# Performance work log

Hardware: AMD Instinct MI355X
Metric: run time of the kernel (lower is better)

The kernel has to match this reference:

```python
import jax, jax.numpy as jnp
import numpy as np

HIDDEN = 1024
HEADS = 16
HEAD_DIM = HIDDEN // HEADS
EPS = 1e-5


def setup_inputs() -> dict:
    key = jax.random.key(0)
    ks = jax.random.split(key, 9)
    B, S, H = 2, 2048, HIDDEN
    scale = 1.0 / np.sqrt(H)
    inp = {
        "hidden_states": jax.random.normal(ks[0], (B, S, H), dtype=jnp.float32),
        "Wq": jax.random.normal(ks[1], (H, H), dtype=jnp.float32) * scale,
        "bq": jnp.zeros((H,), jnp.float32),
        "Wk": jax.random.normal(ks[2], (H, H), dtype=jnp.float32) * scale,
        "bk": jnp.zeros((H,), jnp.float32),
        "Wv": jax.random.normal(ks[3], (H, H), dtype=jnp.float32) * scale,
        "bv": jnp.zeros((H,), jnp.float32),
        "Wo": jax.random.normal(ks[4], (H, H), dtype=jnp.float32) * scale,
        "bo": jnp.zeros((H,), jnp.float32),
        "gamma": jnp.ones((H,), jnp.float32),
        "beta": jnp.zeros((H,), jnp.float32),
    }
    return inp


def reference(hidden_states, Wq, bq, Wk, bk, Wv, bv, Wo, bo, gamma, beta):
    B, S, H = hidden_states.shape
    residual = hidden_states

    def shape(x):  # [B,S,H] -> [B,heads,S,head_dim]
        return x.reshape(B, S, HEADS, HEAD_DIM).transpose(0, 2, 1, 3)

    q = shape(hidden_states @ Wq + bq)
    k = shape(hidden_states @ Wk + bk)
    v = shape(hidden_states @ Wv + bv)

    scores = jnp.einsum("bhqd,bhkd->bhqk", q, k) / jnp.sqrt(
        jnp.asarray(HEAD_DIM, hidden_states.dtype))
    probs = jax.nn.softmax(scores, axis=-1)
    context = jnp.einsum("bhqk,bhkd->bhqd", probs, v)
    context = context.transpose(0, 2, 1, 3).reshape(B, S, H)

    output = context @ Wo + bo
    x = output + residual
    mu = jnp.mean(x, axis=-1, keepdims=True)
    var = jnp.mean(jnp.square(x - mu), axis=-1, keepdims=True)
    return (x - mu) * jax.lax.rsqrt(var + EPS) * gamma + beta
```

## Files before the change

kernel.cpp:

```cpp
#include <hip/hip_runtime.h>
#include <hip/hip_bf16.h>
#include <math.h>

#define HIDDEN 1024
#define HEADS 16
#define HEAD_DIM 64
#define EPS 1e-5f

typedef __attribute__((ext_vector_type(8))) short bf16x8;
typedef __attribute__((ext_vector_type(4))) float f32x4;

#if defined(__has_builtin)
#if __has_builtin(__builtin_amdgcn_exp2f)
#define EXP2(x) __builtin_amdgcn_exp2f(x)
#endif
#endif
#ifndef EXP2
#define EXP2(x) exp2f(x)
#endif

#define QSCALE 0.18033688011112042f

__device__ __forceinline__ short f2bf(float f) {
    union { float f; unsigned u; } v; v.f = f;
    unsigned r = v.u + 0x7fffu + ((v.u >> 16) & 1u);
    return (short)(r >> 16);
}

__device__ __forceinline__ void gl_lds16(const void* g, void* l) {
    __builtin_amdgcn_global_load_lds(
        (const __attribute__((address_space(1))) void*)g,
        (__attribute__((address_space(3))) void*)l, 16, 0, 0);
}

__global__ __launch_bounds__(256) void cast_bf16_kernel(
    const float* __restrict__ in, short* __restrict__ out, int n)
{
    int i = (blockIdx.x * 256 + threadIdx.x) * 4;
    if (i >= n) return;
    float4 v = *(const float4*)(in + i);
    short o[4] = { f2bf(v.x), f2bf(v.y), f2bf(v.z), f2bf(v.w) };
    *(uint2*)(out + i) = *(uint2*)o;
}

__global__ __launch_bounds__(256) void wtrans_kernel(
    const float* __restrict__ Wq, const float* __restrict__ Wk,
    const float* __restrict__ Wv, const float* __restrict__ Wo,
    short* __restrict__ Wt3, short* __restrict__ Wot)
{
    const int wsel = blockIdx.z;
    const float* W = (wsel == 0) ? Wq : (wsel == 1) ? Wk : (wsel == 2) ? Wv : Wo;
    short* dst = (wsel < 3) ? (Wt3 + (size_t)wsel * 1024 * 1024) : Wot;
    const float scale = (wsel == 0) ? QSCALE : 1.0f;

    __shared__ short tile[32][33];
    int n0 = blockIdx.x * 32;
    int k0 = blockIdx.y * 32;
    int tx = threadIdx.x & 31;
    int ty = threadIdx.x >> 5;
    #pragma unroll
    for (int i = 0; i < 32; i += 8)
        tile[ty + i][tx] = f2bf(W[(size_t)(k0 + ty + i) * 1024 + n0 + tx] * scale);
    __syncthreads();
    #pragma unroll
    for (int i = 0; i < 32; i += 8)
        dst[(size_t)(n0 + ty + i) * 1024 + k0 + tx] = tile[tx][ty + i];
}

__global__ __launch_bounds__(256) void concat_bias_kernel(
    const float* __restrict__ bq, const float* __restrict__ bk,
    const float* __restrict__ bv, float* __restrict__ b3)
{
    int i = blockIdx.x * 256 + threadIdx.x;
    if (i >= 3072) return;
    float v = (i < 1024) ? bq[i] * QSCALE
            : (i < 2048) ? bk[i - 1024] : bv[i - 2048];
    b3[i] = v;
}

__global__ __launch_bounds__(256) void gemm_bt_mfma(
    const short* __restrict__ A, const short* __restrict__ Bt,
    const float* __restrict__ bias,
    void* __restrict__ C0, int ldc0,
    void* __restrict__ C1, int split_col, int ldc1,
    const float* __restrict__ resid,
    int M, int N, int K, int out_bf16)
{
    __shared__ short As[128 * 32];
    __shared__ short Bs[128 * 32];
    const int tid = threadIdx.x;
    const int wave = tid >> 6, lane = tid & 63;
    const int ln16 = lane & 15, quad = lane >> 4;
    const int wm = (wave >> 1) * 64, wn = (wave & 1) * 64;
    const int brow = blockIdx.y * 128, bcol = blockIdx.x * 128;

    const int sr  = lane >> 2;
    const int scb = lane & 3;

    f32x4 acc[4][4];
    #pragma unroll
    for (int mt = 0; mt < 4; ++mt)
        #pragma unroll
        for (int nt = 0; nt < 4; ++nt) acc[mt][nt] = (f32x4){0.f, 0.f, 0.f, 0.f};

    for (int k0 = 0; k0 < K; k0 += 32) {
        __syncthreads();
        #pragma unroll
        for (int i = 0; i < 2; ++i) {
            int rb = i * 64 + wave * 16;
            int r  = rb + sr;
            int csrc = (scb ^ ((r >> 1) & 3)) * 8;
            gl_lds16(A  + (size_t)(brow + r) * K + k0 + csrc, &As[rb * 32]);
            gl_lds16(Bt + (size_t)(bcol + r) * K + k0 + csrc, &Bs[rb * 32]);
        }
        __syncthreads();

        bf16x8 af[4], bf[4];
        #pragma unroll
        for (int mt = 0; mt < 4; ++mt) {
            int r = wm + mt * 16 + ln16;
            af[mt] = *(const bf16x8*)&As[r * 32 + ((quad ^ ((r >> 1) & 3)) * 8)];
        }
        #pragma unroll
        for (int nt = 0; nt < 4; ++nt) {
            int r = wn + nt * 16 + ln16;
            bf[nt] = *(const bf16x8*)&Bs[r * 32 + ((quad ^ ((r >> 1) & 3)) * 8)];
        }
        #pragma unroll
        for (int mt = 0; mt < 4; ++mt)
            #pragma unroll
            for (int nt = 0; nt < 4; ++nt)
                acc[mt][nt] = __builtin_amdgcn_mfma_f32_16x16x32_bf16(
                    af[mt], bf[nt], acc[mt][nt], 0, 0, 0);
    }

    void* Cp = C0; int ld = ldc0; int coff = 0;
    if (bcol >= split_col) { Cp = C1; ld = ldc1; coff = split_col; }

    #pragma unroll
    for (int mt = 0; mt < 4; ++mt) {
        #pragma unroll
        for (int r = 0; r < 4; ++r) {
            int row = brow + wm + mt * 16 + quad * 4 + r;
            #pragma unroll
            for (int nt = 0; nt < 4; ++nt) {
                int col = bcol + wn + nt * 16 + ln16;
                float v = acc[mt][nt][r] + bias[col];
                if (resid) v += resid[(size_t)row * N + col];
                if (out_bf16) ((short*)Cp)[(size_t)row * ld + (col - coff)] = f2bf(v);
                else          ((float*)Cp)[(size_t)row * ld + (col - coff)] = v;
            }
        }
    }
}

__global__ __launch_bounds__(256) void vtranspose_kernel(
    const short* __restrict__ Vb, short* __restrict__ VT)
{
    __shared__ short t[64][72];
    const int c0 = blockIdx.x * 64;
    const int r0 = blockIdx.y * 64;
    const int tid = threadIdx.x;
    #pragma unroll
    for (int i = 0; i < 2; ++i) {
        int idx = tid + i * 256;
        int r = idx >> 3, cc = (idx & 7) * 8;
        *(uint4*)&t[r][cc] = *(const uint4*)(Vb + (size_t)(r0 + r) * 1024 + c0 + cc);
    }
    __syncthreads();
    #pragma unroll
    for (int i = 0; i < 2; ++i) {
        int idx = tid + i * 256;
        int c = idx >> 3, rr = (idx & 7) * 8;
        short tmp[8];
        #pragma unroll
        for (int j = 0; j < 8; ++j) tmp[j] = t[rr + j][c];
        *(uint4*)(VT + (size_t)(c0 + c) * 4096 + r0 + rr) = *(uint4*)tmp;
    }
}

__global__ __launch_bounds__(256) void attn_mfma_kernel(
    const short* __restrict__ QKb, const short* __restrict__ VT,
    short* __restrict__ Ctx)
{
    const int S = 2048;
    const int h = blockIdx.x, qt = blockIdx.y, b = blockIdx.z;
    const int tid = threadIdx.x;
    const int wave = tid >> 6, lane = tid & 63;
    const int ln16 = lane & 15, quad = lane >> 4;

    __shared__ short Ks[64 * 64];
    __shared__ short Vs[64 * 64];
    __shared__ short Ps[128 * 72];

    const int q0 = qt * 128 + wave * 32;

    bf16x8 qfrag[2][2];
    #pragma unroll
    for (int qg = 0; qg < 2; ++qg)
        #pragma unroll
        for (int kb = 0; kb < 2; ++kb)
            qfrag[qg][kb] = *(const bf16x8*)(QKb +
                (size_t)(b * S + q0 + qg * 16 + ln16) * 2048 + h * 64 + kb * 32 + quad * 8);

    bf16x8 ones;
    #pragma unroll
    for (int j = 0; j < 8; ++j) ones[j] = (short)0x3F80;

    f32x4 of[2][4], lacc[2];
    #pragma unroll
    for (int qg = 0; qg < 2; ++qg) {
        lacc[qg] = (f32x4){0.f, 0.f, 0.f, 0.f};
        #pragma unroll
        for (int nt = 0; nt < 4; ++nt) of[qg][nt] = (f32x4){0.f, 0.f, 0.f, 0.f};
    }

    const int sr  = lane >> 3;
    const int scb = lane & 7;

    for (int kt = 0; kt < S / 64; ++kt) {
        __syncthreads();
        #pragma unroll
        for (int i = 0; i < 2; ++i) {
            int ci = wave * 2 + i;
            int r  = ci * 8 + sr;
            int csrc = ((scb ^ (r & 7))) * 8;
            gl_lds16(QKb + (size_t)(b * S + kt * 64 + r) * 2048 + 1024 + h * 64 + csrc,
                     &Ks[ci * 512]);
            gl_lds16(VT + (size_t)(h * 64 + r) * 4096 + b * S + kt * 64 + csrc,
                     &Vs[ci * 512]);
        }
        __syncthreads();

        #pragma unroll
        for (int nt = 0; nt < 4; ++nt) {
            bf16x8 kf[2];
            #pragma unroll
            for (int kb = 0; kb < 2; ++kb) {
                int r = nt * 16 + ln16;
                int cb = (kb * 4 + quad) ^ (r & 7);
                kf[kb] = *(const bf16x8*)&Ks[r * 64 + cb * 8];
            }
            #pragma unroll
            for (int qg = 0; qg < 2; ++qg) {
                f32x4 a = (f32x4){0.f, 0.f, 0.f, 0.f};
                a = __builtin_amdgcn_mfma_f32_16x16x32_bf16(kf[0], qfrag[qg][0], a, 0, 0, 0);
                a = __builtin_amdgcn_mfma_f32_16x16x32_bf16(kf[1], qfrag[qg][1], a, 0, 0, 0);
                float p0 = EXP2(a[0]), p1 = EXP2(a[1]);
                float p2 = EXP2(a[2]), p3 = EXP2(a[3]);
                union { __hip_bfloat162 h2; unsigned u; } c01, c23;
                c01.h2 = __float22bfloat162_rn(make_float2(p0, p1));
                c23.h2 = __float22bfloat162_rn(make_float2(p2, p3));
                uint2 w; w.x = c01.u; w.y = c23.u;
                *(uint2*)&Ps[(wave * 32 + qg * 16 + ln16) * 72 + nt * 16 + quad * 4] = w;
            }
        }

        bf16x8 pf[2][2];
        #pragma unroll
        for (int qg = 0; qg < 2; ++qg)
            #pragma unroll
            for (int kb = 0; kb < 2; ++kb)
                pf[qg][kb] = *(const bf16x8*)
                    &Ps[(wave * 32 + qg * 16 + ln16) * 72 + kb * 32 + quad * 8];

        #pragma unroll
        for (int qg = 0; qg < 2; ++qg) {
            lacc[qg] = __builtin_amdgcn_mfma_f32_16x16x32_bf16(pf[qg][0], ones, lacc[qg], 0, 0, 0);
            lacc[qg] = __builtin_amdgcn_mfma_f32_16x16x32_bf16(pf[qg][1], ones, lacc[qg], 0, 0, 0);
        }
        #pragma unroll
        for (int nt = 0; nt < 4; ++nt) {
            bf16x8 vf[2];
            #pragma unroll
            for (int kb = 0; kb < 2; ++kb) {
                int r = nt * 16 + ln16;
                int cb = (kb * 4 + quad) ^ (r & 7);
                vf[kb] = *(const bf16x8*)&Vs[r * 64 + cb * 8];
            }
            #pragma unroll
            for (int qg = 0; qg < 2; ++qg) {
                of[qg][nt] = __builtin_amdgcn_mfma_f32_16x16x32_bf16(pf[qg][0], vf[0], of[qg][nt], 0, 0, 0);
                of[qg][nt] = __builtin_amdgcn_mfma_f32_16x16x32_bf16(pf[qg][1], vf[1], of[qg][nt], 0, 0, 0);
            }
        }
    }

    #pragma unroll
    for (int qg = 0; qg < 2; ++qg) {
        #pragma unroll
        for (int r = 0; r < 4; ++r) {
            float inv = 1.f / lacc[qg][r];
            int row = b * S + qt * 128 + wave * 32 + qg * 16 + quad * 4 + r;
            #pragma unroll
            for (int nt = 0; nt < 4; ++nt)
                Ctx[(size_t)row * 1024 + h * 64 + nt * 16 + ln16] =
                    f2bf(of[qg][nt][r] * inv);
        }
    }
}

__global__ __launch_bounds__(256) void resln_kernel(
    const float* __restrict__ xin, const float* __restrict__ gamma,
    const float* __restrict__ beta, float* __restrict__ out)
{
    const int row = blockIdx.x;
    const int tid = threadIdx.x;
    const int wid = tid >> 6, lane = tid & 63;
    __shared__ float red[8];

    float4 x = *(const float4*)(xin + (size_t)row * HIDDEN + tid * 4);
    float s = x.x + x.y + x.z + x.w;
    #pragma unroll
    for (int off = 32; off > 0; off >>= 1) s += __shfl_xor(s, off, 64);
    if (lane == 0) red[wid] = s;
    __syncthreads();
    float mu = (red[0] + red[1] + red[2] + red[3]) * (1.f / HIDDEN);

    float dx = x.x - mu, dy = x.y - mu, dz = x.z - mu, dw = x.w - mu;
    float v = dx * dx + dy * dy + dz * dz + dw * dw;
    #pragma unroll
    for (int off = 32; off > 0; off >>= 1) v += __shfl_xor(v, off, 64);
    if (lane == 0) red[4 + wid] = v;
    __syncthreads();
    float var = (red[4] + red[5] + red[6] + red[7]) * (1.f / HIDDEN);
    float rstd = rsqrtf(var + EPS);

    float4 g = *(const float4*)(gamma + tid * 4);
    float4 bt = *(const float4*)(beta + tid * 4);
    float4 o;
    o.x = dx * rstd * g.x + bt.x;
    o.y = dy * rstd * g.y + bt.y;
    o.z = dz * rstd * g.z + bt.z;
    o.w = dw * rstd * g.w + bt.w;
    *(float4*)(out + (size_t)row * HIDDEN + tid * 4) = o;
}

extern "C" void kernel_launch(void* const* d_in, const int* in_sizes, int n_in,
                              void* d_out, int out_size, void* d_ws, size_t ws_size,
                              hipStream_t stream)
{
    const float* X     = (const float*)d_in[0];
    const float* Wq    = (const float*)d_in[1];
    const float* bq    = (const float*)d_in[2];
    const float* Wk    = (const float*)d_in[3];
    const float* bk    = (const float*)d_in[4];
    const float* Wv    = (const float*)d_in[5];
    const float* bv    = (const float*)d_in[6];
    const float* Wo    = (const float*)d_in[7];
    const float* bo    = (const float*)d_in[8];
    const float* gamma = (const float*)d_in[9];
    const float* beta  = (const float*)d_in[10];
    float* out = (float*)d_out;

    const int B = 2, S = 2048;
    const int M = B * S;
    const size_t mat = (size_t)M * HIDDEN;

    char* ws = (char*)d_ws;
    short* Xb  = (short*)(ws);
    short* VT  = (short*)(ws);
    short* Wot = (short*)(ws + (8ull << 20));
    short* Wt3 = (short*)(ws + (10ull << 20));
    float* b3  = (float*)(ws + (16ull << 20));
    short* QKb = (short*)(ws + (17ull << 20));
    float* Pj  = (float*)(ws + (17ull << 20));
    short* Vb  = (short*)(ws + (33ull << 20));
    short* Ctx = (short*)(ws + (33ull << 20));

    dim3 blk(256);

    cast_bf16_kernel<<<dim3((int)(mat / 4 / 256)), blk, 0, stream>>>(X, Xb, (int)mat);
    wtrans_kernel<<<dim3(32, 32, 4), blk, 0, stream>>>(Wq, Wk, Wv, Wo, Wt3, Wot);
    concat_bias_kernel<<<12, blk, 0, stream>>>(bq, bk, bv, b3);

    dim3 qkvgrid(3072 / 128, M / 128);
    gemm_bt_mfma<<<qkvgrid, blk, 0, stream>>>(Xb, Wt3, b3,
                                              QKb, 2048, Vb, 2048, 1024,
                                              nullptr, M, 3072, HIDDEN, 1);

    vtranspose_kernel<<<dim3(16, 64), blk, 0, stream>>>(Vb, VT);

    dim3 agrid(HEADS, S / 128, B);
    attn_mfma_kernel<<<agrid, blk, 0, stream>>>(QKb, VT, Ctx);

    dim3 ogrid(HIDDEN / 128, M / 128);
    gemm_bt_mfma<<<ogrid, blk, 0, stream>>>(Ctx, Wot, bo,
                                            Pj, 1024, nullptr, 1 << 30, 0,
                                            X, M, HIDDEN, HIDDEN, 0);

    resln_kernel<<<M, blk, 0, stream>>>(Pj, gamma, beta, out);
}
```

Baseline: 245.7 us.

## Double-buffer K/V tiles and halve attention query tile per block

The attention kernel now double-buffers the K and V shared-memory tiles, prefetching the next tile with async global-to-LDS loads while the current one is computed, and replaces the two __syncthreads with explicit vmcnt waits and barriers. Each block now covers 64 queries (16 per wave) instead of 128, which doubles the grid and cuts per-thread registers so more blocks fit per CU. The P scratch buffer uses an XOR swizzle in place of padding to avoid bank conflicts. In exchange, every K/V tile is loaded twice as often across the grid, so global/L2 traffic rises.

```diff
diff --git a/kernel.cpp b/kernel.cpp
--- a/kernel.cpp
+++ b/kernel.cpp
@@ -179,58 +179,72 @@
     }
 }
 
-__global__ __launch_bounds__(256) void attn_mfma_kernel(
+__global__ __launch_bounds__(256, 4) void attn_mfma_kernel(
     const short* __restrict__ QKb, const short* __restrict__ VT,
     short* __restrict__ Ctx)
 {
     const int S = 2048;
+    const int NT = S / 64;
     const int h = blockIdx.x, qt = blockIdx.y, b = blockIdx.z;
     const int tid = threadIdx.x;
     const int wave = tid >> 6, lane = tid & 63;
     const int ln16 = lane & 15, quad = lane >> 4;
 
-    __shared__ short Ks[64 * 64];
-    __shared__ short Vs[64 * 64];
-    __shared__ short Ps[128 * 72];
-
-    const int q0 = qt * 128 + wave * 32;
-
-    bf16x8 qfrag[2][2];
-    #pragma unroll
-    for (int qg = 0; qg < 2; ++qg)
-        #pragma unroll
-        for (int kb = 0; kb < 2; ++kb)
-            qfrag[qg][kb] = *(const bf16x8*)(QKb +
-                (size_t)(b * S + q0 + qg * 16 + ln16) * 2048 + h * 64 + kb * 32 + quad * 8);
+    __shared__ short Ks[2][64 * 64];
+    __shared__ short Vs[2][64 * 64];
+    __shared__ short Ps[64 * 64];
+
+    const int q0 = qt * 64 + wave * 16;
+
+    bf16x8 qfrag[2];
+    #pragma unroll
+    for (int kb = 0; kb < 2; ++kb)
+        qfrag[kb] = *(const bf16x8*)(QKb +
+            (size_t)(b * S + q0 + ln16) * 2048 + h * 64 + kb * 32 + quad * 8);
 
     bf16x8 ones;
     #pragma unroll
     for (int j = 0; j < 8; ++j) ones[j] = (short)0x3F80;
 
-    f32x4 of[2][4], lacc[2];
-    #pragma unroll
-    for (int qg = 0; qg < 2; ++qg) {
-        lacc[qg] = (f32x4){0.f, 0.f, 0.f, 0.f};
-        #pragma unroll
-        for (int nt = 0; nt < 4; ++nt) of[qg][nt] = (f32x4){0.f, 0.f, 0.f, 0.f};
-    }
+    f32x4 of[4], lacc = (f32x4){0.f, 0.f, 0.f, 0.f};
+    #pragma unroll
+    for (int nt = 0; nt < 4; ++nt) of[nt] = (f32x4){0.f, 0.f, 0.f, 0.f};
 
     const int sr  = lane >> 3;
     const int scb = lane & 7;
 
-    for (int kt = 0; kt < S / 64; ++kt) {
-        __syncthreads();
+    auto stage = [&](int p, int kt) {
         #pragma unroll
         for (int i = 0; i < 2; ++i) {
             int ci = wave * 2 + i;
             int r  = ci * 8 + sr;
             int csrc = ((scb ^ (r & 7))) * 8;
             gl_lds16(QKb + (size_t)(b * S + kt * 64 + r) * 2048 + 1024 + h * 64 + csrc,
-                     &Ks[ci * 512]);
+                     &Ks[p][ci * 512]);
             gl_lds16(VT + (size_t)(h * 64 + r) * 4096 + b * S + kt * 64 + csrc,
-                     &Vs[ci * 512]);
-        }
-        __syncthreads();
+                     &Vs[p][ci * 512]);
+        }
+    };
+
+    const int prow = wave * 16 + ln16;
+    const int pkey = prow & 7;
+
+    stage(0, 0);
+
+    for (int kt = 0; kt < NT; ++kt) {
+        const int p = kt & 1;
+
+        if (kt + 1 < NT) {
+            stage(p ^ 1, kt + 1);
+            asm volatile("s_waitcnt vmcnt(4)" ::: "memory");
+        } else {
+            asm volatile("s_waitcnt vmcnt(0)" ::: "memory");
+        }
+        __builtin_amdgcn_s_barrier();
+        __builtin_amdgcn_sched_barrier(0);
+
+        const short* ks = Ks[p];
+        const short* vs = Vs[p];
 
         #pragma unroll
         for (int nt = 0; nt < 4; ++nt) {
@@ -239,36 +253,32 @@
             for (int kb = 0; kb < 2; ++kb) {
                 int r = nt * 16 + ln16;
                 int cb = (kb * 4 + quad) ^ (r & 7);
-                kf[kb] = *(const bf16x8*)&Ks[r * 64 + cb * 8];
+                kf[kb] = *(const bf16x8*)&ks[r * 64 + cb * 8];
             }
-            #pragma unroll
-            for (int qg = 0; qg < 2; ++qg) {
-                f32x4 a = (f32x4){0.f, 0.f, 0.f, 0.f};
-                a = __builtin_amdgcn_mfma_f32_16x16x32_bf16(kf[0], qfrag[qg][0], a, 0, 0, 0);
-                a = __builtin_amdgcn_mfma_f32_16x16x32_bf16(kf[1], qfrag[qg][1], a, 0, 0, 0);
-                float p0 = EXP2(a[0]), p1 = EXP2(a[1]);
-                float p2 = EXP2(a[2]), p3 = EXP2(a[3]);
-                union { __hip_bfloat162 h2; unsigned u; } c01, c23;
-                c01.h2 = __float22bfloat162_rn(make_float2(p0, p1));
-                c23.h2 = __float22bfloat162_rn(make_float2(p2, p3));
-                uint2 w; w.x = c01.u; w.y = c23.u;
-                *(uint2*)&Ps[(wave * 32 + qg * 16 + ln16) * 72 + nt * 16 + quad * 4] = w;
-            }
-        }
-
-        bf16x8 pf[2][2];
-        #pragma unroll
-        for (int qg = 0; qg < 2; ++qg)
-            #pragma unroll
-            for (int kb = 0; kb < 2; ++kb)
-                pf[qg][kb] = *(const bf16x8*)
-                    &Ps[(wave * 32 + qg * 16 + ln16) * 72 + kb * 32 + quad * 8];
-
-        #pragma unroll
-        for (int qg = 0; qg < 2; ++qg) {
-            lacc[qg] = __builtin_amdgcn_mfma_f32_16x16x32_bf16(pf[qg][0], ones, lacc[qg], 0, 0, 0);
-            lacc[qg] = __builtin_amdgcn_mfma_f32_16x16x32_bf16(pf[qg][1], ones, lacc[qg], 0, 0, 0);
-        }
+            f32x4 a = (f32x4){0.f, 0.f, 0.f, 0.f};
+            a = __builtin_amdgcn_mfma_f32_16x16x32_bf16(kf[0], qfrag[0], a, 0, 0, 0);
+            a = __builtin_amdgcn_mfma_f32_16x16x32_bf16(kf[1], qfrag[1], a, 0, 0, 0);
+            float p0 = EXP2(a[0]), p1 = EXP2(a[1]);
+            float p2 = EXP2(a[2]), p3 = EXP2(a[3]);
+            union { __hip_bfloat162 h2; unsigned u; } c01, c23;
+            c01.h2 = __float22bfloat162_rn(make_float2(p0, p1));
+            c23.h2 = __float22bfloat162_rn(make_float2(p2, p3));
+            uint2 w; w.x = c01.u; w.y = c23.u;
+            int c16 = nt * 2 + (quad >> 1);
+            int cby = ((c16 ^ pkey) << 4) | ((quad & 1) << 3);
+            *(uint2*)((char*)Ps + prow * 128 + cby) = w;
+        }
+
+        bf16x8 pf[2];
+        #pragma unroll
+        for (int kb = 0; kb < 2; ++kb) {
+            int c16 = (kb * 4 + quad) ^ pkey;
+            pf[kb] = *(const bf16x8*)((const char*)Ps + prow * 128 + (c16 << 4));
+        }
+
+        lacc = __builtin_amdgcn_mfma_f32_16x16x32_bf16(pf[0], ones, lacc, 0, 0, 0);
+        lacc = __builtin_amdgcn_mfma_f32_16x16x32_bf16(pf[1], ones, lacc, 0, 0, 0);
+
         #pragma unroll
         for (int nt = 0; nt < 4; ++nt) {
             bf16x8 vf[2];
@@ -276,27 +286,24 @@
             for (int kb = 0; kb < 2; ++kb) {
                 int r = nt * 16 + ln16;
                 int cb = (kb * 4 + quad) ^ (r & 7);
-                vf[kb] = *(const bf16x8*)&Vs[r * 64 + cb * 8];
+                vf[kb] = *(const bf16x8*)&vs[r * 64 + cb * 8];
             }
-            #pragma unroll
-            for (int qg = 0; qg < 2; ++qg) {
-                of[qg][nt] = __builtin_amdgcn_mfma_f32_16x16x32_bf16(pf[qg][0], vf[0], of[qg][nt], 0, 0, 0);
-                of[qg][nt] = __builtin_amdgcn_mfma_f32_16x16x32_bf16(pf[qg][1], vf[1], of[qg][nt], 0, 0, 0);
-            }
-        }
-    }
-
-    #pragma unroll
-    for (int qg = 0; qg < 2; ++qg) {
-        #pragma unroll
-        for (int r = 0; r < 4; ++r) {
-            float inv = 1.f / lacc[qg][r];
-            int row = b * S + qt * 128 + wave * 32 + qg * 16 + quad * 4 + r;
-            #pragma unroll
-            for (int nt = 0; nt < 4; ++nt)
-                Ctx[(size_t)row * 1024 + h * 64 + nt * 16 + ln16] =
-                    f2bf(of[qg][nt][r] * inv);
-        }
+            of[nt] = __builtin_amdgcn_mfma_f32_16x16x32_bf16(pf[0], vf[0], of[nt], 0, 0, 0);
+            of[nt] = __builtin_amdgcn_mfma_f32_16x16x32_bf16(pf[1], vf[1], of[nt], 0, 0, 0);
+        }
+
+        __builtin_amdgcn_sched_barrier(0);
+        __builtin_amdgcn_s_barrier();
+    }
+
+    #pragma unroll
+    for (int r = 0; r < 4; ++r) {
+        float inv = 1.f / lacc[r];
+        int row = b * S + qt * 64 + wave * 16 + quad * 4 + r;
+        #pragma unroll
+        for (int nt = 0; nt < 4; ++nt)
+            Ctx[(size_t)row * 1024 + h * 64 + nt * 16 + ln16] =
+                f2bf(of[nt][r] * inv);
     }
 }
 
@@ -381,7 +388,7 @@
 
     vtranspose_kernel<<<dim3(16, 64), blk, 0, stream>>>(Vb, VT);
 
-    dim3 agrid(HEADS, S / 128, B);
+    dim3 agrid(HEADS, S / 64, B);
     attn_mfma_kernel<<<agrid, blk, 0, stream>>>(QKb, VT, Ctx);
 
     dim3 ogrid(HIDDEN / 128, M / 128);
```

Result: slower. 251.1 us (+2.2%).

## Split attention key range across waves and reduce partial outputs in LDS

Applied to the files above, without the earlier changes.

The attention kernel now gives each block 64 queries. Each wave handles a quarter of the key sequence for all 64 queries, loading K and V fragments straight from global memory instead of staging shared tiles behind barriers. Partial output accumulators and row sums are merged through LDS at the end, and the grid doubles along the query dimension. This removes per-tile block syncs and LDS staging, at the cost of uncoalesced direct global loads, more registers per wave, and a final cross-wave reduction.

```diff
diff --git a/kernel.cpp b/kernel.cpp
--- a/kernel.cpp
+++ b/kernel.cpp
@@ -179,7 +179,7 @@
     }
 }
 
-__global__ __launch_bounds__(256) void attn_mfma_kernel(
+__global__ __launch_bounds__(256, 3) void attn_mfma_kernel(
     const short* __restrict__ QKb, const short* __restrict__ VT,
     short* __restrict__ Ctx)
 {
@@ -189,114 +189,118 @@
     const int wave = tid >> 6, lane = tid & 63;
     const int ln16 = lane & 15, quad = lane >> 4;
 
-    __shared__ short Ks[64 * 64];
-    __shared__ short Vs[64 * 64];
-    __shared__ short Ps[128 * 72];
-
-    const int q0 = qt * 128 + wave * 32;
-
-    bf16x8 qfrag[2][2];
-    #pragma unroll
-    for (int qg = 0; qg < 2; ++qg)
+    __shared__ alignas(16) char smem[20480];
+    char* Pw = smem + wave * 4096;
+
+    bf16x8 qf[4][2];
+    #pragma unroll
+    for (int qg = 0; qg < 4; ++qg)
         #pragma unroll
         for (int kb = 0; kb < 2; ++kb)
-            qfrag[qg][kb] = *(const bf16x8*)(QKb +
-                (size_t)(b * S + q0 + qg * 16 + ln16) * 2048 + h * 64 + kb * 32 + quad * 8);
+            qf[qg][kb] = *(const bf16x8*)(QKb +
+                (size_t)(b * S + qt * 64 + qg * 16 + ln16) * 2048 +
+                h * 64 + kb * 32 + quad * 8);
 
     bf16x8 ones;
     #pragma unroll
     for (int j = 0; j < 8; ++j) ones[j] = (short)0x3F80;
 
-    f32x4 of[2][4], lacc[2];
-    #pragma unroll
-    for (int qg = 0; qg < 2; ++qg) {
+    f32x4 of[4][4], lacc[4];
+    #pragma unroll
+    for (int qg = 0; qg < 4; ++qg) {
         lacc[qg] = (f32x4){0.f, 0.f, 0.f, 0.f};
         #pragma unroll
         for (int nt = 0; nt < 4; ++nt) of[qg][nt] = (f32x4){0.f, 0.f, 0.f, 0.f};
     }
 
-    const int sr  = lane >> 3;
-    const int scb = lane & 7;
-
-    for (int kt = 0; kt < S / 64; ++kt) {
-        __syncthreads();
-        #pragma unroll
-        for (int i = 0; i < 2; ++i) {
-            int ci = wave * 2 + i;
-            int r  = ci * 8 + sr;
-            int csrc = ((scb ^ (r & 7))) * 8;
-            gl_lds16(QKb + (size_t)(b * S + kt * 64 + r) * 2048 + 1024 + h * 64 + csrc,
-                     &Ks[ci * 512]);
-            gl_lds16(VT + (size_t)(h * 64 + r) * 4096 + b * S + kt * 64 + csrc,
-                     &Vs[ci * 512]);
-        }
-        __syncthreads();
-
-        #pragma unroll
-        for (int nt = 0; nt < 4; ++nt) {
-            bf16x8 kf[2];
-            #pragma unroll
-            for (int kb = 0; kb < 2; ++kb) {
-                int r = nt * 16 + ln16;
-                int cb = (kb * 4 + quad) ^ (r & 7);
-                kf[kb] = *(const bf16x8*)&Ks[r * 64 + cb * 8];
-            }
-            #pragma unroll
-            for (int qg = 0; qg < 2; ++qg) {
+    const short* Kbase = QKb + (size_t)b * S * 2048 + 1024 + h * 64;
+    const short* Vbase = VT + (size_t)(h * 64) * 4096 + (size_t)b * S;
+
+    #pragma unroll 1
+    for (int it = 0; it < 16; ++it) {
+        const int t0 = wave * 512 + it * 32;
+
+        #pragma unroll
+        for (int kblk = 0; kblk < 2; ++kblk) {
+            const short* krow = Kbase + (size_t)(t0 + kblk * 16 + ln16) * 2048;
+            bf16x8 kf0 = *(const bf16x8*)(krow + quad * 8);
+            bf16x8 kf1 = *(const bf16x8*)(krow + 32 + quad * 8);
+            #pragma unroll
+            for (int qg = 0; qg < 4; ++qg) {
                 f32x4 a = (f32x4){0.f, 0.f, 0.f, 0.f};
-                a = __builtin_amdgcn_mfma_f32_16x16x32_bf16(kf[0], qfrag[qg][0], a, 0, 0, 0);
-                a = __builtin_amdgcn_mfma_f32_16x16x32_bf16(kf[1], qfrag[qg][1], a, 0, 0, 0);
+                a = __builtin_amdgcn_mfma_f32_16x16x32_bf16(kf0, qf[qg][0], a, 0, 0, 0);
+                a = __builtin_amdgcn_mfma_f32_16x16x32_bf16(kf1, qf[qg][1], a, 0, 0, 0);
                 float p0 = EXP2(a[0]), p1 = EXP2(a[1]);
                 float p2 = EXP2(a[2]), p3 = EXP2(a[3]);
                 union { __hip_bfloat162 h2; unsigned u; } c01, c23;
                 c01.h2 = __float22bfloat162_rn(make_float2(p0, p1));
                 c23.h2 = __float22bfloat162_rn(make_float2(p2, p3));
                 uint2 w; w.x = c01.u; w.y = c23.u;
-                *(uint2*)&Ps[(wave * 32 + qg * 16 + ln16) * 72 + nt * 16 + quad * 4] = w;
+                int row = qg * 16 + ln16;
+                int blk = (kblk * 2 + (quad >> 1)) ^ (row & 3);
+                *(uint2*)(Pw + row * 64 + blk * 16 + (quad & 1) * 8) = w;
             }
         }
 
-        bf16x8 pf[2][2];
-        #pragma unroll
-        for (int qg = 0; qg < 2; ++qg)
-            #pragma unroll
-            for (int kb = 0; kb < 2; ++kb)
-                pf[qg][kb] = *(const bf16x8*)
-                    &Ps[(wave * 32 + qg * 16 + ln16) * 72 + kb * 32 + quad * 8];
-
-        #pragma unroll
-        for (int qg = 0; qg < 2; ++qg) {
-            lacc[qg] = __builtin_amdgcn_mfma_f32_16x16x32_bf16(pf[qg][0], ones, lacc[qg], 0, 0, 0);
-            lacc[qg] = __builtin_amdgcn_mfma_f32_16x16x32_bf16(pf[qg][1], ones, lacc[qg], 0, 0, 0);
+        bf16x8 pf[4];
+        #pragma unroll
+        for (int qg = 0; qg < 4; ++qg) {
+            int row = qg * 16 + ln16;
+            int blk = quad ^ (row & 3);
+            pf[qg] = *(const bf16x8*)(Pw + row * 64 + blk * 16);
+            lacc[qg] = __builtin_amdgcn_mfma_f32_16x16x32_bf16(pf[qg], ones, lacc[qg], 0, 0, 0);
         }
         #pragma unroll
         for (int nt = 0; nt < 4; ++nt) {
-            bf16x8 vf[2];
-            #pragma unroll
-            for (int kb = 0; kb < 2; ++kb) {
-                int r = nt * 16 + ln16;
-                int cb = (kb * 4 + quad) ^ (r & 7);
-                vf[kb] = *(const bf16x8*)&Vs[r * 64 + cb * 8];
-            }
-            #pragma unroll
-            for (int qg = 0; qg < 2; ++qg) {
-                of[qg][nt] = __builtin_amdgcn_mfma_f32_16x16x32_bf16(pf[qg][0], vf[0], of[qg][nt], 0, 0, 0);
-                of[qg][nt] = __builtin_amdgcn_mfma_f32_16x16x32_bf16(pf[qg][1], vf[1], of[qg][nt], 0, 0, 0);
-            }
-        }
-    }
-
-    #pragma unroll
-    for (int qg = 0; qg < 2; ++qg) {
-        #pragma unroll
-        for (int r = 0; r < 4; ++r) {
-            float inv = 1.f / lacc[qg][r];
-            int row = b * S + qt * 128 + wave * 32 + qg * 16 + quad * 4 + r;
-            #pragma unroll
-            for (int nt = 0; nt < 4; ++nt)
-                Ctx[(size_t)row * 1024 + h * 64 + nt * 16 + ln16] =
-                    f2bf(of[qg][nt][r] * inv);
-        }
+            bf16x8 vf = *(const bf16x8*)(Vbase + (size_t)(nt * 16 + ln16) * 4096 + t0 + quad * 8);
+            #pragma unroll
+            for (int qg = 0; qg < 4; ++qg)
+                of[qg][nt] = __builtin_amdgcn_mfma_f32_16x16x32_bf16(pf[qg], vf, of[qg][nt], 0, 0, 0);
+        }
+    }
+
+    __syncthreads();
+
+    float* Rw = (float*)(smem + wave * 4864);
+    float* Lb = (float*)(smem + 4 * 4864);
+
+    if (ln16 == 0) {
+        #pragma unroll
+        for (int qg = 0; qg < 4; ++qg)
+            #pragma unroll
+            for (int r = 0; r < 4; ++r)
+                Lb[wave * 64 + qg * 16 + quad * 4 + r] = lacc[qg][r];
+    }
+
+    const int rq  = tid >> 2;
+    const int rd0 = (tid & 3) * 4;
+    float inv = 0.f;
+
+    #pragma unroll
+    for (int nt = 0; nt < 4; ++nt) {
+        #pragma unroll
+        for (int qg = 0; qg < 4; ++qg)
+            #pragma unroll
+            for (int r = 0; r < 4; ++r)
+                Rw[(qg * 16 + quad * 4 + r) * 19 + ln16] = of[qg][nt][r];
+        __syncthreads();
+        if (nt == 0) {
+            float l = Lb[rq] + Lb[64 + rq] + Lb[128 + rq] + Lb[192 + rq];
+            inv = 1.f / l;
+        }
+        short o4[4];
+        #pragma unroll
+        for (int j = 0; j < 4; ++j) {
+            int d = rd0 + j;
+            float s = 0.f;
+            #pragma unroll
+            for (int w = 0; w < 4; ++w)
+                s += ((const float*)(smem + w * 4864))[rq * 19 + d];
+            o4[j] = f2bf(s * inv);
+        }
+        *(uint2*)(Ctx + (size_t)(b * S + qt * 64 + rq) * 1024 + h * 64 + nt * 16 + rd0) =
+            *(uint2*)o4;
+        __syncthreads();
     }
 }
 
@@ -381,7 +385,7 @@
 
     vtranspose_kernel<<<dim3(16, 64), blk, 0, stream>>>(Vb, VT);
 
-    dim3 agrid(HEADS, S / 128, B);
+    dim3 agrid(HEADS, S / 64, B);
     attn_mfma_kernel<<<agrid, blk, 0, stream>>>(QKb, VT, Ctx);
 
     dim3 ogrid(HIDDEN / 128, M / 128);
```

After: 261.3 us. 1.06x slower.
